# Kernel tuning notes

Measured on AMD Instinct MI355X. Metric: run time of the kernel, lower is better.

Reference implementation:

```python
import jax, jax.numpy as jnp
import numpy as np

# Each of the 16 soft logic gates in tableOperator is a polynomial
#   gate_t(A,B) = c0 + cA*A + cB*B + cAB*A*B
# _COEFF[t] = [c0, cA, cB, cAB], matching the torch tableOperator rows 0..15.
_COEFF = np.array([
    [0,  0,  0,  0],   # 0: 0
    [0,  0,  0,  1],   # 1: A*B
    [0,  1,  0, -1],   # 2: A - A*B
    [0,  1,  0,  0],   # 3: A
    [0,  0,  1, -1],   # 4: B - A*B
    [0,  0,  1,  0],   # 5: B
    [0,  1,  1, -2],   # 6: A + B - 2AB
    [0,  1,  1, -1],   # 7: A + B - AB
    [1, -1, -1,  1],   # 8: 1 - (A + B - AB)
    [1, -1, -1,  2],   # 9: 1 - (A + B - 2AB)
    [1,  0, -1,  0],   # 10: 1 - B
    [1,  0, -1,  1],   # 11: 1 - B + AB
    [1, -1,  0,  0],   # 12: 1 - A
    [1, -1,  0,  1],   # 13: 1 - A + AB
    [1,  0,  0, -1],   # 14: 1 - AB
    [1,  0,  0,  0],   # 15: 1
], dtype=np.float32)

PREV_SIZE, SIZE, BATCH = 2048, 2048, 8192

def setup_inputs() -> dict:
    key = jax.random.key(0)
    k1, k2, k3, k4 = jax.random.split(key, 4)
    return {
        "prev_layer_output": jax.random.uniform(k1, (PREV_SIZE, BATCH), dtype=jnp.float32),
        "input_A_weights": jax.random.normal(k2, (SIZE, PREV_SIZE), dtype=jnp.float32) * 0.05,
        "input_B_weights": jax.random.normal(k3, (SIZE, PREV_SIZE), dtype=jnp.float32) * 0.05,
        "table_weights": jax.random.normal(k4, (16, SIZE), dtype=jnp.float32) * 0.05,
    }

def reference(prev_layer_output, input_A_weights, input_B_weights, table_weights):
    # Training (grad-enabled) path of LogicLayer.forward; GradFactor(x, 1) is identity.
    pA = jax.nn.softmax(input_A_weights, axis=1)   # [size, prev_size]
    pB = jax.nn.softmax(input_B_weights, axis=1)   # [size, prev_size]
    pT = jax.nn.softmax(table_weights, axis=0)     # [16, size]
    A = pA @ prev_layer_output                     # [size, batch]
    B = pB @ prev_layer_output                     # [size, batch]
    # Fuse sum_t pT[t] * gate_t(A,B): contract gate coefficients with table probs.
    c = jnp.einsum('tc,ts->cs', jnp.asarray(_COEFF), pT)  # [4, size]
    out = (c[0][:, None]
           + c[1][:, None] * A
           + c[2][:, None] * B
           + c[3][:, None] * (A * B))               # [size, batch]
    return out
```

## Files before the change

### kernel.cpp

```cpp
#include <hip/hip_runtime.h>
#include <hip/hip_bf16.h>

#define M_DIM 2048
#define K_DIM 2048
#define N_DIM 8192

#define BM 128
#define BN 256
#define BK 128
#define NT (K_DIM / BK)

typedef __attribute__((ext_vector_type(4))) int i32x4;

static __device__ __forceinline__ void stage1k(const unsigned char* g, void* l) {
    __builtin_amdgcn_global_load_lds(
        (const __attribute__((address_space(1))) void*)g,
        (__attribute__((address_space(3))) void*)l, 16, 0, 0);
}

__global__ __launch_bounds__(256) void softmax_rows_kernel(
    const float* __restrict__ Wa, const float* __restrict__ Wb,
    unsigned char* __restrict__ Pa, unsigned char* __restrict__ Pb,
    float* __restrict__ SA, float* __restrict__ SB)
{
    const float* W = blockIdx.y ? Wb : Wa;
    unsigned char* P = blockIdx.y ? Pb : Pa;
    float* S = blockIdx.y ? SB : SA;
    const int row = blockIdx.x;
    const int t = threadIdx.x;
    const float* w = W + (size_t)row * K_DIM + t * 8;
    float4 v0 = *(const float4*)(w);
    float4 v1 = *(const float4*)(w + 4);
    float x[8] = {v0.x, v0.y, v0.z, v0.w, v1.x, v1.y, v1.z, v1.w};

    float m = x[0];
#pragma unroll
    for (int i = 1; i < 8; ++i) m = fmaxf(m, x[i]);
#pragma unroll
    for (int off = 32; off >= 1; off >>= 1) m = fmaxf(m, __shfl_xor(m, off));
    __shared__ float redm[4], reds[4];
    const int wid = t >> 6;
    if ((t & 63) == 0) redm[wid] = m;
    __syncthreads();
    m = fmaxf(fmaxf(redm[0], redm[1]), fmaxf(redm[2], redm[3]));

    float s = 0.f;
#pragma unroll
    for (int i = 0; i < 8; ++i) { x[i] = __expf(x[i] - m); s += x[i]; }
#pragma unroll
    for (int off = 32; off >= 1; off >>= 1) s += __shfl_xor(s, off);
    if ((t & 63) == 0) reds[wid] = s;
    __syncthreads();
    s = reds[0] + reds[1] + reds[2] + reds[3];

    union { unsigned char u[8]; int2 v; } pk;
#pragma unroll
    for (int i = 0; i < 8; ++i)
        pk.u[i] = (unsigned char)(int)(127.f * x[i] + 0.5f);
    *(int2*)(P + (size_t)row * K_DIM + t * 8) = pk.v;
    if (t == 0) S[row] = 1.f / (16129.f * s);
}

__global__ __launch_bounds__(256) void table_c_kernel(
    const float* __restrict__ TW, float4* __restrict__ C4)
{
    const int s = blockIdx.x * 256 + threadIdx.x;
    if (s >= M_DIM) return;
    float x[16];
    float m = -1e30f;
#pragma unroll
    for (int t = 0; t < 16; ++t) { x[t] = TW[t * M_DIM + s]; m = fmaxf(m, x[t]); }
    float sum = 0.f;
#pragma unroll
    for (int t = 0; t < 16; ++t) { x[t] = __expf(x[t] - m); sum += x[t]; }
    const float inv = 1.0f / sum;

    const float c0a[16] = {0,0,0,0,0,0,0,0, 1,1,1,1,1,1,1,1};
    const float cAa[16] = {0,0,1,1,0,0,1,1, -1,-1,0,0,-1,-1,0,0};
    const float cBa[16] = {0,0,0,0,1,1,1,1, -1,-1,-1,-1,0,0,0,0};
    const float cXa[16] = {0,1,-1,0,-1,0,-2,-1, 1,2,0,1,0,1,-1,0};
    float c0 = 0.f, cA = 0.f, cB = 0.f, cX = 0.f;
#pragma unroll
    for (int t = 0; t < 16; ++t) {
        const float p = x[t] * inv;
        c0 += p * c0a[t]; cA += p * cAa[t]; cB += p * cBa[t]; cX += p * cXa[t];
    }
    C4[s] = make_float4(c0, cA, cB, cX);
}

__global__ __launch_bounds__(256) void transp_conv_kernel(
    const float* __restrict__ src, unsigned char* __restrict__ dst)
{
    __shared__ unsigned char tile[64][80];
    const int n0 = blockIdx.x * 64;
    const int k0 = blockIdx.y * 64;
    const int t = threadIdx.x;
    const int kb = (t >> 4) * 4;
    const int nb = (t & 15) * 4;

    unsigned int pk0 = 0, pk1 = 0, pk2 = 0, pk3 = 0;
#pragma unroll
    for (int j = 0; j < 4; ++j) {
        float4 v = *(const float4*)(src + (size_t)(k0 + kb + j) * N_DIM + n0 + nb);
        pk0 |= (unsigned int)(unsigned char)(int)(127.f * v.x + 0.5f) << (8 * j);
        pk1 |= (unsigned int)(unsigned char)(int)(127.f * v.y + 0.5f) << (8 * j);
        pk2 |= (unsigned int)(unsigned char)(int)(127.f * v.z + 0.5f) << (8 * j);
        pk3 |= (unsigned int)(unsigned char)(int)(127.f * v.w + 0.5f) << (8 * j);
    }
    *(unsigned int*)&tile[nb + 0][kb] = pk0;
    *(unsigned int*)&tile[nb + 1][kb] = pk1;
    *(unsigned int*)&tile[nb + 2][kb] = pk2;
    *(unsigned int*)&tile[nb + 3][kb] = pk3;
    __syncthreads();
    const int n = t >> 2;
    const int k16 = (t & 3) * 16;
    int4 v = *(const int4*)&tile[n][k16];
    *(int4*)(dst + (size_t)(n0 + n) * K_DIM + k0 + k16) = v;
}


#define MFMA8(ACC, FA, FP, MI0)                                                \
    _Pragma("unroll") for (int mi = (MI0); mi < (MI0) + 2; ++mi)               \
    _Pragma("unroll") for (int ni = 0; ni < 4; ++ni)                           \
        ACC[mi][ni] = __builtin_amdgcn_mfma_i32_16x16x64_i8(                   \
            FA[mi], FP[ni], ACC[mi][ni], 0, 0, 0);

#define STAGE_A(T) do { const int b_ = (T) & 1; const size_t o_ = (size_t)(T) * BK; \
    stage1k(gPa + o_,  &sPa[b_][0][wid * 16][0]);                              \
    stage1k(gPt0 + o_, &sPt[b_][0][wid * 16][0]); } while (0)
#define STAGE_B(T) do { const int b_ = (T) & 1; const size_t o_ = (size_t)(T) * BK; \
    stage1k(gPt1 + o_, &sPt[b_][0][128 + wid * 16][0]);                        \
    stage1k(gPb + o_,  &sPb[b_][0][wid * 16][0]); } while (0)
#define STAGE_C(T) do { const int b_ = (T) & 1; const size_t o_ = (size_t)(T) * BK + 64; \
    stage1k(gPa + o_,  &sPa[b_][1][wid * 16][0]);                              \
    stage1k(gPt0 + o_, &sPt[b_][1][wid * 16][0]); } while (0)
#define STAGE_D(T) do { const int b_ = (T) & 1; const size_t o_ = (size_t)(T) * BK + 64; \
    stage1k(gPt1 + o_, &sPt[b_][1][128 + wid * 16][0]);                        \
    stage1k(gPb + o_,  &sPb[b_][1][wid * 16][0]); } while (0)

__global__ __launch_bounds__(512, 2) void logic_gemm_kernel(
    const unsigned char* __restrict__ Pa,
    const unsigned char* __restrict__ Pb,
    const unsigned char* __restrict__ Pt,
    const float4* __restrict__ C4,
    const float* __restrict__ SA,
    const float* __restrict__ SB,
    float* __restrict__ out)
{
    __shared__ unsigned char sPa[2][2][128][64];
    __shared__ unsigned char sPb[2][2][128][64];
    __shared__ unsigned char sPt[2][2][256][64];

    const int m0 = blockIdx.y * BM;
    const int n0 = blockIdx.x * BN;
    const int t = threadIdx.x;
    const int wid = t >> 6, lane = t & 63;
    const int wr = wid >> 2, wc = wid & 3;
    const int lq = lane >> 4, lr = lane & 15;

    const int srow = lane >> 2;
    const int scol = (((lane & 3) ^ ((lane >> 3) & 3)) << 4);
    const unsigned char* gPa  = Pa + (size_t)(m0 + wid * 16 + srow) * K_DIM + scol;
    const unsigned char* gPb  = Pb + (size_t)(m0 + wid * 16 + srow) * K_DIM + scol;
    const unsigned char* gPt0 = Pt + (size_t)(n0 + wid * 16 + srow) * K_DIM + scol;
    const unsigned char* gPt1 = gPt0 + (size_t)128 * K_DIM;

    const int cswz = (lq ^ ((lr >> 1) & 3)) << 4;
    const int roA = (wr * 64 + lr) * 64 + cswz;
    const int roP = (wc * 64 + lr) * 64 + cswz;

    i32x4 accA[4][4] = {};
    i32x4 accB[4][4] = {};
    i32x4 fX0[4], fX1[4], fpA[4], fpB[4];

    STAGE_A(0); STAGE_B(0); STAGE_C(0); STAGE_D(0);
    STAGE_A(1); STAGE_B(1); STAGE_C(1);
    asm volatile("s_waitcnt vmcnt(10)" ::: "memory");
    __builtin_amdgcn_s_barrier();
#pragma unroll
    for (int i = 0; i < 4; ++i)
        fX0[i] = *(const i32x4*)((const char*)&sPa[0][0][0][0] + roA + i * 1024);
#pragma unroll
    for (int i = 0; i < 4; ++i)
        fpA[i] = *(const i32x4*)((const char*)&sPt[0][0][0][0] + roP + i * 1024);

    for (int kt = 0; kt < NT; ++kt) {
        const int buf = kt & 1;
        const char* bA1 = (const char*)&sPa[buf][1][0][0];
        const char* bB0 = (const char*)&sPb[buf][0][0][0];
        const char* bB1 = (const char*)&sPb[buf][1][0][0];
        const char* bP1 = (const char*)&sPt[buf][1][0][0];
        const char* nA0 = (const char*)&sPa[buf ^ 1][0][0][0];
        const char* nP0 = (const char*)&sPt[buf ^ 1][0][0][0];

        __builtin_amdgcn_s_setprio(1);
        MFMA8(accA, fX0, fpA, 0);
        __builtin_amdgcn_s_setprio(0);
        if (kt < NT - 2) asm volatile("s_waitcnt vmcnt(6)" ::: "memory");
        else             asm volatile("s_waitcnt vmcnt(0)" ::: "memory");
#pragma unroll
        for (int i = 0; i < 4; ++i) fX1[i] = *(const i32x4*)(bB0 + roA + i * 1024);
        if (kt + 1 < NT) STAGE_D(kt + 1);
        __builtin_amdgcn_s_setprio(1);
        MFMA8(accA, fX0, fpA, 2);
        __builtin_amdgcn_s_setprio(0);
        __builtin_amdgcn_s_barrier();

        __builtin_amdgcn_s_setprio(1);
        MFMA8(accB, fX1, fpA, 0);
        __builtin_amdgcn_s_setprio(0);
#pragma unroll
        for (int i = 0; i < 4; ++i) fX0[i] = *(const i32x4*)(bA1 + roA + i * 1024);
#pragma unroll
        for (int i = 0; i < 4; ++i) fpB[i] = *(const i32x4*)(bP1 + roP + i * 1024);
        if (kt + 2 < NT) STAGE_A(kt + 2);
        __builtin_amdgcn_s_setprio(1);
        MFMA8(accB, fX1, fpA, 2);
        __builtin_amdgcn_s_setprio(0);
        __builtin_amdgcn_s_barrier();

        __builtin_amdgcn_s_setprio(1);
        MFMA8(accA, fX0, fpB, 0);
        __builtin_amdgcn_s_setprio(0);
        if (kt < NT - 2) asm volatile("s_waitcnt vmcnt(6)" ::: "memory");
        else             asm volatile("s_waitcnt vmcnt(0)" ::: "memory");
#pragma unroll
        for (int i = 0; i < 4; ++i) fX1[i] = *(const i32x4*)(bB1 + roA + i * 1024);
        if (kt + 2 < NT) STAGE_B(kt + 2);
        __builtin_amdgcn_s_setprio(1);
        MFMA8(accA, fX0, fpB, 2);
        __builtin_amdgcn_s_setprio(0);
        __builtin_amdgcn_s_barrier();

        __builtin_amdgcn_s_setprio(1);
        MFMA8(accB, fX1, fpB, 0);
        __builtin_amdgcn_s_setprio(0);
#pragma unroll
        for (int i = 0; i < 4; ++i) fX0[i] = *(const i32x4*)(nA0 + roA + i * 1024);
#pragma unroll
        for (int i = 0; i < 4; ++i) fpA[i] = *(const i32x4*)(nP0 + roP + i * 1024);
        if (kt + 2 < NT) STAGE_C(kt + 2);
        __builtin_amdgcn_s_setprio(1);
        MFMA8(accB, fX1, fpB, 2);
        __builtin_amdgcn_s_setprio(0);
        __builtin_amdgcn_s_barrier();
    }

#pragma unroll
    for (int mi = 0; mi < 4; ++mi) {
#pragma unroll
        for (int i = 0; i < 4; ++i) {
            const int row = m0 + wr * 64 + mi * 16 + lq * 4 + i;
            const float4 c = C4[row];
            const float sa = SA[row];
            const float sb = SB[row];
#pragma unroll
            for (int ni = 0; ni < 4; ++ni) {
                const int col = n0 + wc * 64 + ni * 16 + lr;
                const float Av = (float)accA[mi][ni][i] * sa;
                const float Bv = (float)accB[mi][ni][i] * sb;
                out[(size_t)row * N_DIM + col] = c.x + c.y * Av + c.z * Bv + c.w * Av * Bv;
            }
        }
    }
}

extern "C" void kernel_launch(void* const* d_in, const int* in_sizes, int n_in,
                              void* d_out, int out_size, void* d_ws, size_t ws_size,
                              hipStream_t stream) {
    const float* prev = (const float*)d_in[0];
    const float* Wa   = (const float*)d_in[1];
    const float* Wb   = (const float*)d_in[2];
    const float* TW   = (const float*)d_in[3];
    float* out = (float*)d_out;

    char* ws = (char*)d_ws;
    unsigned char* Pa = (unsigned char*)(ws);
    unsigned char* Pb = (unsigned char*)(ws + (size_t)(4u << 20));
    unsigned char* Pt = (unsigned char*)(ws + (size_t)(8u << 20));
    float4* C4 = (float4*)(ws + (size_t)(24u << 20));
    float*  SA = (float*)(ws + (size_t)(24u << 20) + (32u << 10));
    float*  SB = (float*)(ws + (size_t)(24u << 20) + (64u << 10));

    softmax_rows_kernel<<<dim3(2048, 2), 256, 0, stream>>>(Wa, Wb, Pa, Pb, SA, SB);
    table_c_kernel<<<dim3(8), 256, 0, stream>>>(TW, C4);
    transp_conv_kernel<<<dim3(N_DIM / 64, K_DIM / 64), 256, 0, stream>>>(prev, Pt);
    logic_gemm_kernel<<<dim3(N_DIM / BN, M_DIM / BM), 512, 0, stream>>>(Pa, Pb, Pt, C4, SA, SB, out);
}
```

Before: 89.53 us.

## Merge prep kernels into one launch and restructure GEMM LDS pipeline to half-tile stages

Combines the row-softmax, table-coefficient and transpose/quantize kernels into a single prep kernel dispatched by block index, removing two launches and the gaps between them. The int8 GEMM main loop is rescheduled: each K-half now loads A, B and P fragments together into double-buffered register sets, and global-to-LDS staging is grouped per half (A+B, then C+D), giving two barriers per K-tile instead of four. This cuts synchronisation but raises register pressure (six fragment arrays) and changes how global loads overlap with MFMA work.

```diff
diff --git a/kernel.cpp b/kernel.cpp
--- a/kernel.cpp
+++ b/kernel.cpp
@@ -18,104 +18,103 @@
         (__attribute__((address_space(3))) void*)l, 16, 0, 0);
 }
 
-__global__ __launch_bounds__(256) void softmax_rows_kernel(
-    const float* __restrict__ Wa, const float* __restrict__ Wb,
+__global__ __launch_bounds__(256) void prep_kernel(
+    const float* __restrict__ prev, const float* __restrict__ Wa,
+    const float* __restrict__ Wb, const float* __restrict__ TW,
     unsigned char* __restrict__ Pa, unsigned char* __restrict__ Pb,
-    float* __restrict__ SA, float* __restrict__ SB)
+    unsigned char* __restrict__ Pt,
+    float* __restrict__ SA, float* __restrict__ SB, float4* __restrict__ C4)
 {
-    const float* W = blockIdx.y ? Wb : Wa;
-    unsigned char* P = blockIdx.y ? Pb : Pa;
-    float* S = blockIdx.y ? SB : SA;
-    const int row = blockIdx.x;
+    __shared__ unsigned char tile[64][80];
+    __shared__ float redm[4], reds[4];
+    const int bx = blockIdx.x;
     const int t = threadIdx.x;
-    const float* w = W + (size_t)row * K_DIM + t * 8;
-    float4 v0 = *(const float4*)(w);
-    float4 v1 = *(const float4*)(w + 4);
-    float x[8] = {v0.x, v0.y, v0.z, v0.w, v1.x, v1.y, v1.z, v1.w};
-
-    float m = x[0];
-#pragma unroll
-    for (int i = 1; i < 8; ++i) m = fmaxf(m, x[i]);
-#pragma unroll
-    for (int off = 32; off >= 1; off >>= 1) m = fmaxf(m, __shfl_xor(m, off));
-    __shared__ float redm[4], reds[4];
-    const int wid = t >> 6;
-    if ((t & 63) == 0) redm[wid] = m;
-    __syncthreads();
-    m = fmaxf(fmaxf(redm[0], redm[1]), fmaxf(redm[2], redm[3]));
-
-    float s = 0.f;
-#pragma unroll
-    for (int i = 0; i < 8; ++i) { x[i] = __expf(x[i] - m); s += x[i]; }
-#pragma unroll
-    for (int off = 32; off >= 1; off >>= 1) s += __shfl_xor(s, off);
-    if ((t & 63) == 0) reds[wid] = s;
-    __syncthreads();
-    s = reds[0] + reds[1] + reds[2] + reds[3];
-
-    union { unsigned char u[8]; int2 v; } pk;
-#pragma unroll
-    for (int i = 0; i < 8; ++i)
-        pk.u[i] = (unsigned char)(int)(127.f * x[i] + 0.5f);
-    *(int2*)(P + (size_t)row * K_DIM + t * 8) = pk.v;
-    if (t == 0) S[row] = 1.f / (16129.f * s);
-}
-
-__global__ __launch_bounds__(256) void table_c_kernel(
-    const float* __restrict__ TW, float4* __restrict__ C4)
-{
-    const int s = blockIdx.x * 256 + threadIdx.x;
+
+    if (bx < 4096) {
+        const int n0 = (bx & 127) * 64;
+        const int k0 = (bx >> 7) * 64;
+        const int kb = (t >> 4) * 4;
+        const int nb = (t & 15) * 4;
+        unsigned int pk0 = 0, pk1 = 0, pk2 = 0, pk3 = 0;
+#pragma unroll
+        for (int j = 0; j < 4; ++j) {
+            float4 v = *(const float4*)(prev + (size_t)(k0 + kb + j) * N_DIM + n0 + nb);
+            pk0 |= (unsigned int)(unsigned char)(int)(127.f * v.x + 0.5f) << (8 * j);
+            pk1 |= (unsigned int)(unsigned char)(int)(127.f * v.y + 0.5f) << (8 * j);
+            pk2 |= (unsigned int)(unsigned char)(int)(127.f * v.z + 0.5f) << (8 * j);
+            pk3 |= (unsigned int)(unsigned char)(int)(127.f * v.w + 0.5f) << (8 * j);
+        }
+        *(unsigned int*)&tile[nb + 0][kb] = pk0;
+        *(unsigned int*)&tile[nb + 1][kb] = pk1;
+        *(unsigned int*)&tile[nb + 2][kb] = pk2;
+        *(unsigned int*)&tile[nb + 3][kb] = pk3;
+        __syncthreads();
+        const int n = t >> 2;
+        const int k16 = (t & 3) * 16;
+        int4 v = *(const int4*)&tile[n][k16];
+        *(int4*)(Pt + (size_t)(n0 + n) * K_DIM + k0 + k16) = v;
+        return;
+    }
+    if (bx < 8192) {
+        const int r = bx - 4096;
+        const int row = r & 2047;
+        const int isB = r >> 11;
+        const float* W = isB ? Wb : Wa;
+        unsigned char* P = isB ? Pb : Pa;
+        float* S = isB ? SB : SA;
+        const float* w = W + (size_t)row * K_DIM + t * 8;
+        float4 v0 = *(const float4*)(w);
+        float4 v1 = *(const float4*)(w + 4);
+        float x[8] = {v0.x, v0.y, v0.z, v0.w, v1.x, v1.y, v1.z, v1.w};
+
+        float m = x[0];
+#pragma unroll
+        for (int i = 1; i < 8; ++i) m = fmaxf(m, x[i]);
+#pragma unroll
+        for (int off = 32; off >= 1; off >>= 1) m = fmaxf(m, __shfl_xor(m, off));
+        const int wid = t >> 6;
+        if ((t & 63) == 0) redm[wid] = m;
+        __syncthreads();
+        m = fmaxf(fmaxf(redm[0], redm[1]), fmaxf(redm[2], redm[3]));
+
+        float s = 0.f;
+#pragma unroll
+        for (int i = 0; i < 8; ++i) { x[i] = __expf(x[i] - m); s += x[i]; }
+#pragma unroll
+        for (int off = 32; off >= 1; off >>= 1) s += __shfl_xor(s, off);
+        if ((t & 63) == 0) reds[wid] = s;
+        __syncthreads();
+        s = reds[0] + reds[1] + reds[2] + reds[3];
+
+        union { unsigned char u[8]; int2 v; } pk;
+#pragma unroll
+        for (int i = 0; i < 8; ++i)
+            pk.u[i] = (unsigned char)(int)(127.f * x[i] + 0.5f);
+        *(int2*)(P + (size_t)row * K_DIM + t * 8) = pk.v;
+        if (t == 0) S[row] = 1.f / (16129.f * s);
+        return;
+    }
+    const int s = (bx - 8192) * 256 + t;
     if (s >= M_DIM) return;
     float x[16];
     float m = -1e30f;
 #pragma unroll
-    for (int t = 0; t < 16; ++t) { x[t] = TW[t * M_DIM + s]; m = fmaxf(m, x[t]); }
+    for (int tt = 0; tt < 16; ++tt) { x[tt] = TW[tt * M_DIM + s]; m = fmaxf(m, x[tt]); }
     float sum = 0.f;
 #pragma unroll
-    for (int t = 0; t < 16; ++t) { x[t] = __expf(x[t] - m); sum += x[t]; }
+    for (int tt = 0; tt < 16; ++tt) { x[tt] = __expf(x[tt] - m); sum += x[tt]; }
     const float inv = 1.0f / sum;
-
     const float c0a[16] = {0,0,0,0,0,0,0,0, 1,1,1,1,1,1,1,1};
     const float cAa[16] = {0,0,1,1,0,0,1,1, -1,-1,0,0,-1,-1,0,0};
     const float cBa[16] = {0,0,0,0,1,1,1,1, -1,-1,-1,-1,0,0,0,0};
     const float cXa[16] = {0,1,-1,0,-1,0,-2,-1, 1,2,0,1,0,1,-1,0};
     float c0 = 0.f, cA = 0.f, cB = 0.f, cX = 0.f;
 #pragma unroll
-    for (int t = 0; t < 16; ++t) {
-        const float p = x[t] * inv;
-        c0 += p * c0a[t]; cA += p * cAa[t]; cB += p * cBa[t]; cX += p * cXa[t];
+    for (int tt = 0; tt < 16; ++tt) {
+        const float p = x[tt] * inv;
+        c0 += p * c0a[tt]; cA += p * cAa[tt]; cB += p * cBa[tt]; cX += p * cXa[tt];
     }
     C4[s] = make_float4(c0, cA, cB, cX);
-}
-
-__global__ __launch_bounds__(256) void transp_conv_kernel(
-    const float* __restrict__ src, unsigned char* __restrict__ dst)
-{
-    __shared__ unsigned char tile[64][80];
-    const int n0 = blockIdx.x * 64;
-    const int k0 = blockIdx.y * 64;
-    const int t = threadIdx.x;
-    const int kb = (t >> 4) * 4;
-    const int nb = (t & 15) * 4;
-
-    unsigned int pk0 = 0, pk1 = 0, pk2 = 0, pk3 = 0;
-#pragma unroll
-    for (int j = 0; j < 4; ++j) {
-        float4 v = *(const float4*)(src + (size_t)(k0 + kb + j) * N_DIM + n0 + nb);
-        pk0 |= (unsigned int)(unsigned char)(int)(127.f * v.x + 0.5f) << (8 * j);
-        pk1 |= (unsigned int)(unsigned char)(int)(127.f * v.y + 0.5f) << (8 * j);
-        pk2 |= (unsigned int)(unsigned char)(int)(127.f * v.z + 0.5f) << (8 * j);
-        pk3 |= (unsigned int)(unsigned char)(int)(127.f * v.w + 0.5f) << (8 * j);
-    }
-    *(unsigned int*)&tile[nb + 0][kb] = pk0;
-    *(unsigned int*)&tile[nb + 1][kb] = pk1;
-    *(unsigned int*)&tile[nb + 2][kb] = pk2;
-    *(unsigned int*)&tile[nb + 3][kb] = pk3;
-    __syncthreads();
-    const int n = t >> 2;
-    const int k16 = (t & 3) * 16;
-    int4 v = *(const int4*)&tile[n][k16];
-    *(int4*)(dst + (size_t)(n0 + n) * K_DIM + k0 + k16) = v;
 }
 
 
@@ -138,6 +137,14 @@
     stage1k(gPt1 + o_, &sPt[b_][1][128 + wid * 16][0]);                        \
     stage1k(gPb + o_,  &sPb[b_][1][wid * 16][0]); } while (0)
 
+#define RD_SET(FA, FB, FP, BA, BB, BP)                                         \
+    _Pragma("unroll") for (int i = 0; i < 4; ++i)                              \
+        FA[i] = *(const i32x4*)((BA) + roA + i * 1024);                        \
+    _Pragma("unroll") for (int i = 0; i < 4; ++i)                              \
+        FP[i] = *(const i32x4*)((BP) + roP + i * 1024);                        \
+    _Pragma("unroll") for (int i = 0; i < 4; ++i)                              \
+        FB[i] = *(const i32x4*)((BB) + roA + i * 1024);
+
 __global__ __launch_bounds__(512, 2) void logic_gemm_kernel(
     const unsigned char* __restrict__ Pa,
     const unsigned char* __restrict__ Pb,
@@ -171,77 +178,51 @@
 
     i32x4 accA[4][4] = {};
     i32x4 accB[4][4] = {};
-    i32x4 fX0[4], fX1[4], fpA[4], fpB[4];
+    i32x4 fa0[4], fb0[4], fp0[4], fa1[4], fb1[4], fp1[4];
 
     STAGE_A(0); STAGE_B(0); STAGE_C(0); STAGE_D(0);
-    STAGE_A(1); STAGE_B(1); STAGE_C(1);
-    asm volatile("s_waitcnt vmcnt(10)" ::: "memory");
+    STAGE_A(1); STAGE_B(1);
+    asm volatile("s_waitcnt vmcnt(4)" ::: "memory");
     __builtin_amdgcn_s_barrier();
-#pragma unroll
-    for (int i = 0; i < 4; ++i)
-        fX0[i] = *(const i32x4*)((const char*)&sPa[0][0][0][0] + roA + i * 1024);
-#pragma unroll
-    for (int i = 0; i < 4; ++i)
-        fpA[i] = *(const i32x4*)((const char*)&sPt[0][0][0][0] + roP + i * 1024);
+    RD_SET(fa0, fb0, fp0,
+           (const char*)&sPa[0][0][0][0],
+           (const char*)&sPb[0][0][0][0],
+           (const char*)&sPt[0][0][0][0]);
 
     for (int kt = 0; kt < NT; ++kt) {
         const int buf = kt & 1;
         const char* bA1 = (const char*)&sPa[buf][1][0][0];
-        const char* bB0 = (const char*)&sPb[buf][0][0][0];
         const char* bB1 = (const char*)&sPb[buf][1][0][0];
         const char* bP1 = (const char*)&sPt[buf][1][0][0];
         const char* nA0 = (const char*)&sPa[buf ^ 1][0][0][0];
+        const char* nB0 = (const char*)&sPb[buf ^ 1][0][0][0];
         const char* nP0 = (const char*)&sPt[buf ^ 1][0][0][0];
 
         __builtin_amdgcn_s_setprio(1);
-        MFMA8(accA, fX0, fpA, 0);
-        __builtin_amdgcn_s_setprio(0);
-        if (kt < NT - 2) asm volatile("s_waitcnt vmcnt(6)" ::: "memory");
+        MFMA8(accA, fa0, fp0, 0);
+        MFMA8(accA, fa0, fp0, 2);
+        __builtin_amdgcn_s_setprio(0);
+        RD_SET(fa1, fb1, fp1, bA1, bB1, bP1);
+        if (kt + 1 < NT) { STAGE_C(kt + 1); STAGE_D(kt + 1); }
+        if (kt < NT - 1) asm volatile("s_waitcnt vmcnt(4)" ::: "memory");
         else             asm volatile("s_waitcnt vmcnt(0)" ::: "memory");
-#pragma unroll
-        for (int i = 0; i < 4; ++i) fX1[i] = *(const i32x4*)(bB0 + roA + i * 1024);
-        if (kt + 1 < NT) STAGE_D(kt + 1);
-        __builtin_amdgcn_s_setprio(1);
-        MFMA8(accA, fX0, fpA, 2);
+        __builtin_amdgcn_s_setprio(1);
+        MFMA8(accB, fb0, fp0, 0);
+        MFMA8(accB, fb0, fp0, 2);
         __builtin_amdgcn_s_setprio(0);
         __builtin_amdgcn_s_barrier();
 
         __builtin_amdgcn_s_setprio(1);
-        MFMA8(accB, fX1, fpA, 0);
-        __builtin_amdgcn_s_setprio(0);
-#pragma unroll
-        for (int i = 0; i < 4; ++i) fX0[i] = *(const i32x4*)(bA1 + roA + i * 1024);
-#pragma unroll
-        for (int i = 0; i < 4; ++i) fpB[i] = *(const i32x4*)(bP1 + roP + i * 1024);
-        if (kt + 2 < NT) STAGE_A(kt + 2);
-        __builtin_amdgcn_s_setprio(1);
-        MFMA8(accB, fX1, fpA, 2);
-        __builtin_amdgcn_s_setprio(0);
-        __builtin_amdgcn_s_barrier();
-
-        __builtin_amdgcn_s_setprio(1);
-        MFMA8(accA, fX0, fpB, 0);
-        __builtin_amdgcn_s_setprio(0);
-        if (kt < NT - 2) asm volatile("s_waitcnt vmcnt(6)" ::: "memory");
+        MFMA8(accA, fa1, fp1, 0);
+        MFMA8(accA, fa1, fp1, 2);
+        __builtin_amdgcn_s_setprio(0);
+        if (kt + 1 < NT) RD_SET(fa0, fb0, fp0, nA0, nB0, nP0);
+        if (kt + 2 < NT) { STAGE_A(kt + 2); STAGE_B(kt + 2); }
+        if (kt < NT - 2) asm volatile("s_waitcnt vmcnt(4)" ::: "memory");
         else             asm volatile("s_waitcnt vmcnt(0)" ::: "memory");
-#pragma unroll
-        for (int i = 0; i < 4; ++i) fX1[i] = *(const i32x4*)(bB1 + roA + i * 1024);
-        if (kt + 2 < NT) STAGE_B(kt + 2);
-        __builtin_amdgcn_s_setprio(1);
-        MFMA8(accA, fX0, fpB, 2);
-        __builtin_amdgcn_s_setprio(0);
-        __builtin_amdgcn_s_barrier();
-
-        __builtin_amdgcn_s_setprio(1);
-        MFMA8(accB, fX1, fpB, 0);
-        __builtin_amdgcn_s_setprio(0);
-#pragma unroll
-        for (int i = 0; i < 4; ++i) fX0[i] = *(const i32x4*)(nA0 + roA + i * 1024);
-#pragma unroll
-        for (int i = 0; i < 4; ++i) fpA[i] = *(const i32x4*)(nP0 + roP + i * 1024);
-        if (kt + 2 < NT) STAGE_C(kt + 2);
-        __builtin_amdgcn_s_setprio(1);
-        MFMA8(accB, fX1, fpB, 2);
+        __builtin_amdgcn_s_setprio(1);
+        MFMA8(accB, fb1, fp1, 0);
+        MFMA8(accB, fb1, fp1, 2);
         __builtin_amdgcn_s_setprio(0);
         __builtin_amdgcn_s_barrier();
     }
@@ -282,8 +263,7 @@
     float*  SA = (float*)(ws + (size_t)(24u << 20) + (32u << 10));
     float*  SB = (float*)(ws + (size_t)(24u << 20) + (64u << 10));
 
-    softmax_rows_kernel<<<dim3(2048, 2), 256, 0, stream>>>(Wa, Wb, Pa, Pb, SA, SB);
-    table_c_kernel<<<dim3(8), 256, 0, stream>>>(TW, C4);
-    transp_conv_kernel<<<dim3(N_DIM / 64, K_DIM / 64), 256, 0, stream>>>(prev, Pt);
+    prep_kernel<<<dim3(8200), 256, 0, stream>>>(prev, Wa, Wb, TW,
+                                                Pa, Pb, Pt, SA, SB, C4);
     logic_gemm_kernel<<<dim3(N_DIM / BN, M_DIM / BM), 512, 0, stream>>>(Pa, Pb, Pt, C4, SA, SB, out);
 }
```

Result: faster. 83.25 us, median of 2 (-7.0%).
